# Optimization experiments

Hardware: AMD Instinct MI355X
Metric: run time of the kernel (lower is better)

## Reference

```python
import jax, jax.numpy as jnp
import numpy as np

EPS = float(np.finfo(np.float32).eps)


def fake_quant_w(w):
    # per-output-channel symmetric int8 fake quant; w: (out, in)
    w_d = jax.lax.stop_gradient(w)
    max_abs = jnp.max(jnp.abs(w_d), axis=1, keepdims=True)
    scale = jnp.maximum(max_abs / 127.0, EPS)
    w_q = jnp.clip(jnp.round(w_d / scale), -127, 127)
    return w_q * scale


def woq_linear(x, w, b):
    return x @ fake_quant_w(w).T + b


def setup_inputs() -> dict:
    key = jax.random.key(0)
    ks = jax.random.split(key, 9)
    dim = 1024
    B, S = 2, 2048
    def wmat(k):
        return jax.random.normal(k, (dim, dim), dtype=jnp.float32) * (1.0 / np.sqrt(dim))
    def bvec(k):
        return jax.random.normal(k, (dim,), dtype=jnp.float32) * 0.01
    return {
        "x": jax.random.normal(ks[0], (B, S, dim), dtype=jnp.float32),
        "wq": wmat(ks[1]), "bq": bvec(ks[2]),
        "wk": wmat(ks[3]), "bk": bvec(ks[4]),
        "wv": wmat(ks[5]), "bv": bvec(ks[6]),
        "wp": wmat(ks[7]), "bp": bvec(ks[8]),
    }


def reference(x, wq, bq, wk, bk, wv, bv, wp, bp):
    B, S, C = x.shape
    H = 16
    D = C // H
    scale = D ** -0.5
    # QKV projections with fake-quantized weights -> (B, H, S, D)
    q = woq_linear(x, wq, bq).reshape(B, S, H, D).transpose(0, 2, 1, 3)
    k = woq_linear(x, wk, bk).reshape(B, S, H, D).transpose(0, 2, 1, 3)
    v = woq_linear(x, wv, bv).reshape(B, S, H, D).transpose(0, 2, 1, 3)
    attn = jnp.einsum("bhsd,bhtd->bhst", q, k) * scale  # (B,H,S,S)
    attn = jax.nn.softmax(attn, axis=-1)
    out = jnp.einsum("bhst,bhtd->bhsd", attn, v)
    out = out.transpose(0, 2, 1, 3).reshape(B, S, C)
    return woq_linear(out, wp, bp)
```

## Files before the change

kernel.cpp:

```cpp
#include <hip/hip_runtime.h>
#include <stdint.h>

typedef short bf16x8 __attribute__((ext_vector_type(8)));
typedef float f32x4 __attribute__((ext_vector_type(4)));
typedef uint16_t u16;
typedef uint32_t u32;
typedef u16 u16x4 __attribute__((ext_vector_type(4)));

#define EPSF 1.1920929e-07f

static __device__ __forceinline__ u16 f2bf(float f) {
  union { float f; uint32_t u; } v; v.f = f;
  return (u16)((v.u + 0x7FFFu + ((v.u >> 16) & 1u)) >> 16);
}
static __device__ __forceinline__ float bf2f(u16 h) {
  union { uint32_t u; float f; } v; v.u = ((uint32_t)h) << 16;
  return v.f;
}
static __device__ __forceinline__ float exp2_fast(float x) {
  return __builtin_amdgcn_exp2f(x);
}
static __device__ __forceinline__ u32 cvt_pk_bf16(float lo, float hi) {
  u32 r;
  asm("v_cvt_pk_bf16_f32 %0, %1, %2" : "=v"(r) : "v"(lo), "v"(hi));
  return r;
}
static __device__ __forceinline__ void gload_lds16(const void* g, void* l) {
  __builtin_amdgcn_global_load_lds(
      (const __attribute__((address_space(1))) void*)g,
      (__attribute__((address_space(3))) void*)l, 16, 0, 0);
}
template <int N>
static __device__ __forceinline__ void vmwait() {
  asm volatile("s_waitcnt vmcnt(%0)" ::"i"(N) : "memory");
}

__global__ __launch_bounds__(256) void prep_kernel(
    const float* __restrict__ wq, const float* __restrict__ wk,
    const float* __restrict__ wv, const float* __restrict__ wp,
    const float* __restrict__ x,
    u16* __restrict__ wout, float* __restrict__ scales, u16* __restrict__ xb) {
  const int t = threadIdx.x;
  if (blockIdx.x < 4096) {
    const int row = blockIdx.x & 1023;
    const int mat = blockIdx.x >> 10;
    const float* W = (mat == 0) ? wq : (mat == 1) ? wk : (mat == 2) ? wv : wp;
    const float4 v = ((const float4*)(W + (size_t)row * 1024))[t];
    float m = fmaxf(fmaxf(fabsf(v.x), fabsf(v.y)), fmaxf(fabsf(v.z), fabsf(v.w)));
#pragma unroll
    for (int off = 1; off < 64; off <<= 1) m = fmaxf(m, __shfl_xor(m, off));
    __shared__ float red[4];
    if ((t & 63) == 0) red[t >> 6] = m;
    __syncthreads();
    m = fmaxf(fmaxf(red[0], red[1]), fmaxf(red[2], red[3]));
    const float scale = fmaxf(m / 127.0f, EPSF);
    float q0 = fminf(fmaxf(rintf(v.x / scale), -127.f), 127.f);
    float q1 = fminf(fmaxf(rintf(v.y / scale), -127.f), 127.f);
    float q2 = fminf(fmaxf(rintf(v.z / scale), -127.f), 127.f);
    float q3 = fminf(fmaxf(rintf(v.w / scale), -127.f), 127.f);
    u16x4 o; o.x = f2bf(q0); o.y = f2bf(q1); o.z = f2bf(q2); o.w = f2bf(q3);
    *(u16x4*)(wout + ((size_t)(mat * 1024 + row)) * 1024 + t * 4) = o;
    if (t == 0) scales[mat * 1024 + row] = scale;
  } else {
    const int i = (blockIdx.x - 4096) * 256 + t;
    const float4 v = ((const float4*)x)[i];
    u16x4 hv;
    hv.x = f2bf(v.x); hv.y = f2bf(v.y); hv.z = f2bf(v.z); hv.w = f2bf(v.w);
    *(u16x4*)(xb + (size_t)i * 4) = hv;
  }
}

template <int MODE, int MR, int NR, int NT, int KT, int LDA>
__global__ __launch_bounds__(512) void gemm_kernel(
    const u16* __restrict__ A, const u16* __restrict__ Bw,
    const float* __restrict__ scales, const float* __restrict__ b0,
    const float* __restrict__ b1, const float* __restrict__ b2,
    u16* __restrict__ qkv, float* __restrict__ outp) {
  constexpr int BM = 2 * MR * 16;
  constexpr int BN = 4 * NR * 16;
  constexpr int OPS = BM / 64 + BN / 64;
  __shared__ u16 As[2][BM * 64];
  __shared__ u16 Bs[2][BN * 64];
  const int tid = threadIdx.x;
  const int w = tid >> 6, l = tid & 63;
  const int per = gridDim.x >> 3;
  const int L = (blockIdx.x & 7) * per + (blockIdx.x >> 3);
  const int tile_n = (L % NT) * BN;
  const int tile_m = (L / NT) * BM;
  const int wm = w >> 2, wn = w & 3;
  const int l15 = l & 15, l4 = l >> 4;
  const int sw = l15 & 7;

  f32x4 acc[MR][NR];
  const f32x4 vzero = {0.f, 0.f, 0.f, 0.f};
#pragma unroll
  for (int m = 0; m < MR; ++m)
#pragma unroll
    for (int n = 0; n < NR; ++n) acc[m][n] = vzero;

  const int r8 = tid >> 3;
  const int g = tid & 7;
  const int gs = g ^ (r8 & 7);
  auto STAGE = [&](int slot, int j) {
    const int kb = j * 64;
    const int kbB = kb & 1023;
#pragma unroll
    for (int i = 0; i < BM / 64; ++i)
      gload_lds16(A + (size_t)(tile_m + i * 64 + r8) * LDA + kb + gs * 8,
                  &As[slot][(i * 64 + r8) * 64 + g * 8]);
#pragma unroll
    for (int i = 0; i < BN / 64; ++i)
      gload_lds16(Bw + (size_t)(tile_n + i * 64 + r8) * 1024 + kbB + gs * 8,
                  &Bs[slot][(i * 64 + r8) * 64 + g * 8]);
  };

  STAGE(0, 0);
  STAGE(1, 1);
  vmwait<OPS>();
  __builtin_amdgcn_s_barrier();

  for (int j = 0; j < KT; ++j) {
    const int cur = j & 1;
#pragma unroll
    for (int ks = 0; ks < 2; ++ks) {
      bf16x8 af[MR], bfv[NR];
      const int sg8 = ((ks * 4 + l4) ^ sw) * 8;
#pragma unroll
      for (int m = 0; m < MR; ++m)
        af[m] = *(const bf16x8*)(&As[cur][(wm * (MR * 16) + m * 16 + l15) * 64 + sg8]);
#pragma unroll
      for (int n = 0; n < NR; ++n)
        bfv[n] = *(const bf16x8*)(&Bs[cur][(wn * (NR * 16) + n * 16 + l15) * 64 + sg8]);
      __builtin_amdgcn_s_setprio(1);
#pragma unroll
      for (int m = 0; m < MR; ++m)
#pragma unroll
        for (int n = 0; n < NR; ++n)
          acc[m][n] = __builtin_amdgcn_mfma_f32_16x16x32_bf16(af[m], bfv[n], acc[m][n], 0, 0, 0);
      __builtin_amdgcn_s_setprio(0);
    }
    __builtin_amdgcn_s_barrier();
    if (j + 2 < KT) {
      STAGE(cur, j + 2);
      vmwait<OPS>();
    } else {
      vmwait<0>();
    }
    __builtin_amdgcn_s_barrier();
  }

#pragma unroll
  for (int m = 0; m < MR; ++m) {
#pragma unroll
    for (int n = 0; n < NR; ++n) {
      const int col = tile_n + wn * (NR * 16) + n * 16 + l15;
      const float sc = scales[col];
      if constexpr (MODE == 0) {
        const int mat = col >> 10, oo = col & 1023;
        const float* bias = (mat == 0) ? b0 : (mat == 1) ? b1 : b2;
        const float bb = bias[oo];
        const int hh = oo >> 6, dd = oo & 63;
        if (mat == 2) {
          const int rowm0 = tile_m + wm * (MR * 16) + m * 16 + l4 * 4;
          const int b = rowm0 >> 11, s = rowm0 & 2047;
          u16x4 pk;
#pragma unroll
          for (int jj = 0; jj < 4; ++jj) pk[jj] = f2bf(acc[m][n][jj] * sc + bb);
          *(u16x4*)(qkv + (size_t)2 * 4194304 +
                    ((size_t)(b * 16 + hh) * 64 + dd) * 2048 + s) = pk;
        } else {
#pragma unroll
          for (int jj = 0; jj < 4; ++jj) {
            const int rowm = tile_m + wm * (MR * 16) + m * 16 + l4 * 4 + jj;
            const int b = rowm >> 11, s = rowm & 2047;
            float y = acc[m][n][jj] * sc + bb;
            if (mat == 0) y *= 0.18033688011112042f;
            qkv[(size_t)mat * 4194304 + ((size_t)(b * 16 + hh) * 2048 + s) * 64 + dd] = f2bf(y);
          }
        }
      } else {
        const float bb = b0[col];
#pragma unroll
        for (int jj = 0; jj < 4; ++jj) {
          const int rowm = tile_m + wm * (MR * 16) + m * 16 + l4 * 4 + jj;
          outp[(size_t)rowm * 1024 + col] = acc[m][n][jj] * sc + bb;
        }
      }
    }
  }
}

__global__ __launch_bounds__(256, 2) void attn_kernel(
    const u16* __restrict__ qg, const u16* __restrict__ kg,
    const u16* __restrict__ vtg, u16* __restrict__ po) {
  __shared__ u16 Kt[2][128 * 64];
  __shared__ u16 Vt[2][64 * 128];
  __shared__ u16 Pl[4 * 2 * 16 * 64];
  const int tid = threadIdx.x;
  const int w = tid >> 6, l = tid & 63;
  const int Lb = (blockIdx.x & 7) * 64 + (blockIdx.x >> 3);
  const int bh = Lb >> 4;
  const int qt = Lb & 15;
  const u16* qp = qg + (size_t)bh * 131072;
  const u16* kp = kg + (size_t)bh * 131072;
  const u16* vp = vtg + (size_t)bh * 131072;
  const int qrow0 = qt * 128 + w * 32;
  const int l15 = l & 15, l4 = l >> 4;
  const int sw = l15 & 7;

  auto STAGE = [&](const int slot, const int kt) {
#pragma unroll
    for (int i = 0; i < 4; ++i) {
      const int rk = i * 32 + (tid >> 3);
      gload_lds16(kp + (size_t)(kt + rk) * 64 + (((tid & 7) ^ (rk & 7)) << 3),
                  &Kt[slot][i * 2048 + tid * 8]);
    }
#pragma unroll
    for (int i = 0; i < 4; ++i) {
      const int rv = i * 16 + (tid >> 4);
      gload_lds16(vp + (size_t)rv * 2048 + kt + (((tid & 15) ^ (rv & 7)) << 3),
                  &Vt[slot][i * 2048 + tid * 8]);
    }
  };

  bf16x8 qfr[2][2];
#pragma unroll
  for (int dk = 0; dk < 2; ++dk)
#pragma unroll
    for (int qf = 0; qf < 2; ++qf)
      qfr[dk][qf] =
          *(const bf16x8*)(qp + (size_t)(qrow0 + qf * 16 + l15) * 64 + dk * 32 + l4 * 8);

  const f32x4 vzero = {0.f, 0.f, 0.f, 0.f};
  f32x4 O[4][2];
#pragma unroll
  for (int di = 0; di < 4; ++di)
#pragma unroll
    for (int qf = 0; qf < 2; ++qf) O[di][qf] = vzero;
  float lrun[2] = {0.f, 0.f};

  u32* const pb0 = (u32*)Pl + (w * 2 + 0) * 512 + l15 * 32;
  u32* const pb1 = (u32*)Pl + (w * 2 + 1) * 512 + l15 * 32;
  const u16* const pr0 = Pl + (w * 2 + 0) * 1024 + l15 * 64;
  const u16* const pr1 = Pl + (w * 2 + 1) * 1024 + l15 * 64;

  auto DO_ITER = [&](const int slot, const int j) {
    f32x4 sfr[2][8];
#pragma unroll
    for (int qf = 0; qf < 2; ++qf)
#pragma unroll
      for (int ki = 0; ki < 8; ++ki) sfr[qf][ki] = vzero;
#pragma unroll
    for (int dk = 0; dk < 2; ++dk) {
      bf16x8 kf[8];
#pragma unroll
      for (int ki = 0; ki < 8; ++ki)
        kf[ki] = *(const bf16x8*)(&Kt[slot][(ki * 16 + l15) * 64 + (((dk * 4 + l4) ^ sw) << 3)]);
      __builtin_amdgcn_s_setprio(1);
#pragma unroll
      for (int ki = 0; ki < 8; ++ki)
#pragma unroll
        for (int qf = 0; qf < 2; ++qf)
          sfr[qf][ki] = __builtin_amdgcn_mfma_f32_16x16x32_bf16(kf[ki], qfr[dk][qf], sfr[qf][ki], 0, 0, 0);
      __builtin_amdgcn_s_setprio(0);
    }

#pragma unroll
    for (int half = 0; half < 2; ++half) {
      u32 pw[2][8];
#pragma unroll
      for (int qf = 0; qf < 2; ++qf) {
        float rs = 0.f;
#pragma unroll
        for (int ki = 0; ki < 4; ++ki) {
          const f32x4 s4 = sfr[qf][half * 4 + ki];
          const float p0 = exp2_fast(s4[0]);
          const float p1 = exp2_fast(s4[1]);
          const float p2 = exp2_fast(s4[2]);
          const float p3 = exp2_fast(s4[3]);
          rs += (p0 + p1) + (p2 + p3);
          pw[qf][ki * 2 + 0] = cvt_pk_bf16(p0, p1);
          pw[qf][ki * 2 + 1] = cvt_pk_bf16(p2, p3);
        }
        lrun[qf] += rs;
      }
#pragma unroll
      for (int ki = 0; ki < 4; ++ki) {
#pragma unroll
        for (int h = 0; h < 2; ++h) {
          const int W = ki * 8 + l4 * 2 + h;
          const int off = (((W >> 2) ^ sw) << 2) + (W & 3);
          pb0[off] = pw[0][ki * 2 + h];
          pb1[off] = pw[1][ki * 2 + h];
        }
      }

#pragma unroll
      for (int kkl = 0; kkl < 2; ++kkl) {
        bf16x8 pf[2];
        pf[0] = *(const bf16x8*)(pr0 + (((kkl * 4 + l4) ^ sw) << 3));
        pf[1] = *(const bf16x8*)(pr1 + (((kkl * 4 + l4) ^ sw) << 3));
        bf16x8 vf[4];
#pragma unroll
        for (int di = 0; di < 4; ++di)
          vf[di] = *(const bf16x8*)(&Vt[slot][(di * 16 + l15) * 128 +
                                              (((half * 8 + kkl * 4 + l4) ^ sw) << 3)]);
        __builtin_amdgcn_s_setprio(1);
#pragma unroll
        for (int di = 0; di < 4; ++di)
#pragma unroll
          for (int qf = 0; qf < 2; ++qf)
            O[di][qf] = __builtin_amdgcn_mfma_f32_16x16x32_bf16(pf[qf], vf[di], O[di][qf], 0, 0, 0);
        __builtin_amdgcn_s_setprio(0);
      }
    }

    __builtin_amdgcn_s_barrier();
    if (j + 2 < 16) {
      STAGE(slot, (j + 2) * 128);
      vmwait<8>();
    } else {
      vmwait<0>();
    }
    __builtin_amdgcn_s_barrier();
  };

  STAGE(0, 0);
  STAGE(1, 128);
  vmwait<8>();
  __builtin_amdgcn_s_barrier();

  for (int jp = 0; jp < 8; ++jp) {
    DO_ITER(0, jp * 2);
    DO_ITER(1, jp * 2 + 1);
  }

  const int b = bh >> 4, hh = bh & 15;
#pragma unroll
  for (int qf = 0; qf < 2; ++qf) {
    lrun[qf] += __shfl_xor(lrun[qf], 16);
    lrun[qf] += __shfl_xor(lrun[qf], 32);
  }
#pragma unroll
  for (int qf = 0; qf < 2; ++qf) {
    float lq[4];
#pragma unroll
    for (int jj = 0; jj < 4; ++jj)
      lq[jj] = __builtin_amdgcn_rcpf(__shfl(lrun[qf], l4 * 4 + jj));
#pragma unroll
    for (int di = 0; di < 4; ++di)
#pragma unroll
      for (int jj = 0; jj < 4; ++jj) {
        const float oval = O[di][qf][jj] * lq[jj];
        const int srw = qrow0 + qf * 16 + l4 * 4 + jj;
        const int c = hh * 64 + di * 16 + l15;
        po[((size_t)(b * 2048 + srw)) * 1024 + c] = f2bf(oval);
      }
  }
}

extern "C" void kernel_launch(void* const* d_in, const int* in_sizes, int n_in,
                              void* d_out, int out_size, void* d_ws, size_t ws_size,
                              hipStream_t stream) {
  (void)in_sizes; (void)n_in; (void)out_size; (void)ws_size;
  const float* x  = (const float*)d_in[0];
  const float* wq = (const float*)d_in[1];
  const float* bq = (const float*)d_in[2];
  const float* wk = (const float*)d_in[3];
  const float* bk = (const float*)d_in[4];
  const float* wv = (const float*)d_in[5];
  const float* bv = (const float*)d_in[6];
  const float* wp = (const float*)d_in[7];
  const float* bp = (const float*)d_in[8];

  char* ws = (char*)d_ws;
  u16*   wquant = (u16*)ws;
  float* scales = (float*)(ws + 8388608);
  u16*   xb     = (u16*)(ws + 8404992);
  u16*   po     = xb;
  u16*   qkv    = (u16*)(ws + 25182208);

  prep_kernel<<<dim3(8192), dim3(256), 0, stream>>>(
      wq, wk, wv, wp, x, wquant, scales, xb);
  gemm_kernel<0, 4, 3, 16, 16, 1024><<<dim3(512), dim3(512), 0, stream>>>(
      xb, wquant, scales, bq, bk, bv, qkv, nullptr);
  attn_kernel<<<dim3(512), dim3(256), 0, stream>>>(
      qkv, qkv + 4194304, qkv + 8388608, po);
  gemm_kernel<1, 2, 2, 8, 16, 1024><<<dim3(512), dim3(512), 0, stream>>>(
      po, wquant + 3145728, scales + 3072, bp, nullptr, nullptr, nullptr, (float*)d_out);
}
```

Before: 98.69 us.

## Feed P to PV MFMA directly from registers, dropping LDS round-trip

Removes the shared-memory staging buffer for the softmax probabilities P. The packed bf16 values are reinterpreted in registers as MFMA operands. To make that work, the reduction (k) index ordering is permuted, and the V fragments are gathered to match using two 8-byte LDS reads per fragment instead of one 16-byte read. This eliminates the LDS writes and reads of P and frees shared memory, at the cost of more, narrower V reads from LDS.

```diff
diff --git a/kernel.cpp b/kernel.cpp
--- a/kernel.cpp
+++ b/kernel.cpp
@@ -6,6 +6,8 @@
 typedef uint16_t u16;
 typedef uint32_t u32;
 typedef u16 u16x4 __attribute__((ext_vector_type(4)));
+typedef u32 u32x2 __attribute__((ext_vector_type(2)));
+typedef u32 u32x4 __attribute__((ext_vector_type(4)));
 
 #define EPSF 1.1920929e-07f
 
@@ -195,7 +197,6 @@
     const u16* __restrict__ vtg, u16* __restrict__ po) {
   __shared__ u16 Kt[2][128 * 64];
   __shared__ u16 Vt[2][64 * 128];
-  __shared__ u16 Pl[4 * 2 * 16 * 64];
   const int tid = threadIdx.x;
   const int w = tid >> 6, l = tid & 63;
   const int Lb = (blockIdx.x & 7) * 64 + (blockIdx.x >> 3);
@@ -239,11 +240,6 @@
     for (int qf = 0; qf < 2; ++qf) O[di][qf] = vzero;
   float lrun[2] = {0.f, 0.f};
 
-  u32* const pb0 = (u32*)Pl + (w * 2 + 0) * 512 + l15 * 32;
-  u32* const pb1 = (u32*)Pl + (w * 2 + 1) * 512 + l15 * 32;
-  const u16* const pr0 = Pl + (w * 2 + 0) * 1024 + l15 * 64;
-  const u16* const pr1 = Pl + (w * 2 + 1) * 1024 + l15 * 64;
-
   auto DO_ITER = [&](const int slot, const int j) {
     f32x4 sfr[2][8];
 #pragma unroll
@@ -284,33 +280,33 @@
         }
         lrun[qf] += rs;
       }
-#pragma unroll
-      for (int ki = 0; ki < 4; ++ki) {
-#pragma unroll
-        for (int h = 0; h < 2; ++h) {
-          const int W = ki * 8 + l4 * 2 + h;
-          const int off = (((W >> 2) ^ sw) << 2) + (W & 3);
-          pb0[off] = pw[0][ki * 2 + h];
-          pb1[off] = pw[1][ki * 2 + h];
-        }
-      }
 
 #pragma unroll
       for (int kkl = 0; kkl < 2; ++kkl) {
-        bf16x8 pf[2];
-        pf[0] = *(const bf16x8*)(pr0 + (((kkl * 4 + l4) ^ sw) << 3));
-        pf[1] = *(const bf16x8*)(pr1 + (((kkl * 4 + l4) ^ sw) << 3));
+        const int c = half * 2 + kkl;
+        const u32x4 t0 = {pw[0][kkl * 4 + 0], pw[0][kkl * 4 + 1],
+                          pw[0][kkl * 4 + 2], pw[0][kkl * 4 + 3]};
+        const u32x4 t1 = {pw[1][kkl * 4 + 0], pw[1][kkl * 4 + 1],
+                          pw[1][kkl * 4 + 2], pw[1][kkl * 4 + 3]};
+        const bf16x8 pf0 = __builtin_bit_cast(bf16x8, t0);
+        const bf16x8 pf1 = __builtin_bit_cast(bf16x8, t1);
+        const int o0 = (((c * 4 + (l4 >> 1)) ^ sw) << 3) + (l4 & 1) * 4;
+        const int o1 = (((c * 4 + 2 + (l4 >> 1)) ^ sw) << 3) + (l4 & 1) * 4;
         bf16x8 vf[4];
 #pragma unroll
-        for (int di = 0; di < 4; ++di)
-          vf[di] = *(const bf16x8*)(&Vt[slot][(di * 16 + l15) * 128 +
-                                              (((half * 8 + kkl * 4 + l4) ^ sw) << 3)]);
+        for (int di = 0; di < 4; ++di) {
+          const u16* vrow = &Vt[slot][(di * 16 + l15) * 128];
+          const u32x2 lo = *(const u32x2*)(vrow + o0);
+          const u32x2 hi = *(const u32x2*)(vrow + o1);
+          const u32x4 q = {lo.x, lo.y, hi.x, hi.y};
+          vf[di] = __builtin_bit_cast(bf16x8, q);
+        }
         __builtin_amdgcn_s_setprio(1);
 #pragma unroll
-        for (int di = 0; di < 4; ++di)
-#pragma unroll
-          for (int qf = 0; qf < 2; ++qf)
-            O[di][qf] = __builtin_amdgcn_mfma_f32_16x16x32_bf16(pf[qf], vf[di], O[di][qf], 0, 0, 0);
+        for (int di = 0; di < 4; ++di) {
+          O[di][0] = __builtin_amdgcn_mfma_f32_16x16x32_bf16(pf0, vf[di], O[di][0], 0, 0, 0);
+          O[di][1] = __builtin_amdgcn_mfma_f32_16x16x32_bf16(pf1, vf[di], O[di][1], 0, 0, 0);
+        }
         __builtin_amdgcn_s_setprio(0);
       }
     }
```

Result: faster. 96.36 us (-2.4%).
